# Kernel optimization log

Measured on AMD Instinct MI355X. Metric: run time of the kernel, lower is better.

## Reference

```python
import jax, jax.numpy as jnp
import numpy as np

NR, K = 175, 250              # num_ranges, top_k
N = NR * K                    # 43750 active radar points
SHAPE0 = (56, 350, 512)       # (ele, range, azi) full-res sparse grid
SHAPE1 = (28, 175, 256)       # after stride-2 sparse conv
SHAPE2 = (14, 88, 128)        # after second stride-2 sparse conv
CAP1 = 350000                 # <= 8*N unique active cells after stride-2 conv
CAP2 = 69000                  # reachable region bound at stage 2 (14*88*56)
BC = 16                       # base_channel
C1, C2, CO = 2 * BC, 8 * BC, 128
OFFS = [(a, b, c) for a in range(3) for b in range(3) for c in range(3)]


def bn(x, p):
    # BatchNorm1d (eval form): p = [gamma, beta, running_mean, running_var]
    g, b, m, v = p
    return (x - m) * jax.lax.rsqrt(v + 1e-3) * g + b


def gn(x, groups, gamma, beta):
    n, c = x.shape
    xr = x.reshape(n, groups, c // groups)
    m = xr.mean(-1, keepdims=True)
    v = ((xr - m) ** 2).mean(-1, keepdims=True)
    return ((xr - m) * jax.lax.rsqrt(v + 1e-5)).reshape(n, c) * gamma + beta


def build_lut(coords, shape, n):
    # dense coord -> row-index map; out-of-bounds (padded) coords are dropped
    lut = jnp.full(shape, -1, jnp.int32)
    return lut.at[coords[:, 0], coords[:, 1], coords[:, 2]].set(jnp.arange(n, dtype=jnp.int32), mode='drop')


def subm_conv(feats, coords, lut, shape, w):
    # submanifold 3x3x3 conv: outputs only at active sites (gather-GEMM-accumulate)
    S = jnp.array(shape, jnp.int32)
    out = jnp.zeros((feats.shape[0], w.shape[-1]), feats.dtype)
    for k, off in enumerate(OFFS):
        nb = coords + (jnp.array(off, jnp.int32) - 1)
        inb = jnp.all((nb >= 0) & (nb < S), axis=-1)
        nbc = jnp.clip(nb, 0, S - 1)
        idx = lut[nbc[:, 0], nbc[:, 1], nbc[:, 2]]
        ok = inb & (idx >= 0)
        f = jnp.where(ok[:, None], feats[jnp.maximum(idx, 0)], 0.0)
        out = out + f @ w[k]
    return out


def down_conv(feats, coords_in, lut_in, shape_in, shape_out, cap, w):
    # SparseConv3d k=3 stride=2 pad=1: output sites = cells with any active input in receptive field
    mask = jnp.zeros(shape_in, bool).at[coords_in[:, 0], coords_in[:, 1], coords_in[:, 2]].set(True, mode='drop')
    pm = jnp.pad(mask, 1)
    om = jnp.zeros(shape_out, bool)
    for (a, b, c) in OFFS:
        om = om | pm[a:a + 2 * shape_out[0]:2, b:b + 2 * shape_out[1]:2, c:c + 2 * shape_out[2]:2]
    i0, i1, i2 = jnp.nonzero(om, size=cap, fill_value=0)
    oc = jnp.stack([i0, i1, i2], -1).astype(jnp.int32)
    valid = jnp.arange(cap) < om.sum()
    S = jnp.array(shape_in, jnp.int32)
    out = jnp.zeros((cap, w.shape[-1]), feats.dtype)
    for k, off in enumerate(OFFS):
        nb = 2 * oc + (jnp.array(off, jnp.int32) - 1)   # input coord = 2j + k - 1
        inb = jnp.all((nb >= 0) & (nb < S), axis=-1)
        nbc = jnp.clip(nb, 0, S - 1)
        idx = lut_in[nbc[:, 0], nbc[:, 1], nbc[:, 2]]
        ok = inb & (idx >= 0)
        f = jnp.where(ok[:, None], feats[jnp.maximum(idx, 0)], 0.0)
        out = out + f @ w[k]
    # padded (invalid) rows get out-of-bounds coords so later scatters/luts drop them
    oc_safe = jnp.where(valid[:, None], oc, jnp.array(shape_out, jnp.int32))
    return out, oc_safe


def basic_block(f, coords, lut, shape, w2, p2):
    h = jax.nn.relu(bn(subm_conv(f, coords, lut, shape, w2[0]), p2[0]))
    h = bn(subm_conv(h, coords, lut, shape, w2[1]), p2[1])
    return jax.nn.relu(h + f)


def range_attn(pw, c1, c3, ele_table, azi_table, wq, bq, wk, bk, wv, bv):
    x = pw.reshape(NR, K, 1)
    e = ele_table[c1.reshape(NR, K)]   # [NR,K,3]
    a = azi_table[c3.reshape(NR, K)]   # [NR,K,3]
    scale = 32.0 ** -0.5               # queries.size(-1) = hidden_dim = 32
    for l in range(4):
        xin = jnp.concatenate([x, e, a], -1)           # [NR,K,7]
        q = xin @ wq[l] + bq[l]
        kk = xin @ wk[l] + bk[l]
        v = xin @ wv[l] + bv[l]
        att = jax.nn.softmax(jnp.einsum('rkd,rjd->rkj', q, kk) * scale, axis=-1)
        x = jnp.einsum('rkj,rjd->rkd', att, v)         # [NR,K,1]
    return x.reshape(N, 1)


def forward(voxel_features, coors, ele_table, azi_table, wq, bq, wk, bk, wv, bv,
            w_in, b_in, gin_g, gin_b, w_d1, bn_d1, w_r1, bn_r1,
            w_d2, bn_d2, w_r2, bn_r2, w_out, b_out, gout_g, gout_b):
    c1, c2, c3 = coors[:, 1], coors[:, 2], coors[:, 3]
    pw = jnp.log10(voxel_features[:, -2])[:, None]
    f_att = range_attn(pw, c1, c3, ele_table, azi_table, wq, bq, wk, bk, wv, bv)
    ele = c1 * 2 - 9          # (56 - 37*2)//2 = -9
    rng = c2 * 2
    azi = c3 * 2 + 149        # (512 - 107*2)//2 = 149
    feats = jnp.concatenate([ele[:, None].astype(jnp.float32), rng[:, None].astype(jnp.float32),
                             azi[:, None].astype(jnp.float32), f_att], -1)   # [N,4]
    coords0 = jnp.stack([ele, rng, azi], -1).astype(jnp.int32)
    # conv_input: 1x1x1 SubMConv (per-point linear) + GroupNorm(8) + ReLU
    f0 = jax.nn.relu(gn(feats @ w_in + b_in, 8, gin_g, gin_b))
    lut0 = build_lut(coords0, SHAPE0, N)
    f1, oc1 = down_conv(f0, coords0, lut0, SHAPE0, SHAPE1, CAP1, w_d1)
    f1 = jax.nn.relu(bn(f1, bn_d1))
    lut1 = build_lut(oc1, SHAPE1, CAP1)
    f1 = basic_block(f1, oc1, lut1, SHAPE1, w_r1[0], bn_r1[0])
    f1 = basic_block(f1, oc1, lut1, SHAPE1, w_r1[1], bn_r1[1])
    f2, oc2 = down_conv(f1, oc1, lut1, SHAPE1, SHAPE2, CAP2, w_d2)
    f2 = jax.nn.relu(bn(f2, bn_d2))
    lut2 = build_lut(oc2, SHAPE2, CAP2)
    f2 = basic_block(f2, oc2, lut2, SHAPE2, w_r2[0], bn_r2[0])
    f2 = basic_block(f2, oc2, lut2, SHAPE2, w_r2[1], bn_r2[1])
    # conv_out: SubMConv3d(k=3, bias) + GroupNorm(16) + ReLU
    fo = subm_conv(f2, oc2, lut2, SHAPE2, w_out) + b_out
    fo = jax.nn.relu(gn(fo, 16, gout_g, gout_b))
    dense = jnp.zeros(SHAPE2 + (CO,), fo.dtype).at[oc2[:, 0], oc2[:, 1], oc2[:, 2]].set(fo, mode='drop')
    # torch dense: [1,C,ele,range,azi].permute(0,1,4,3,2) -> [1,C,azi,range,ele]
    return jnp.transpose(dense, (3, 2, 1, 0))[None]


def setup_inputs():
    key = jax.random.key(0)
    ks = iter(jax.random.split(key, 64))
    nrm = lambda shp, s: jax.random.normal(next(ks), shp, jnp.float32) * s

    def bnp(c):
        return jnp.stack([1.0 + nrm((c,), 0.1), nrm((c,), 0.1), nrm((c,), 0.05),
                          1.0 + 0.1 * jax.random.uniform(next(ks), (c,), jnp.float32)])

    voxel_features = jax.random.uniform(next(ks), (N, 2), jnp.float32, 0.1, 100.0)
    c0 = jnp.zeros((N,), jnp.int32)
    c1 = jax.random.randint(next(ks), (N,), 5, 33, jnp.int32)      # ele bin -> ele_ind in [1,55]
    c2 = jnp.repeat(jnp.arange(NR, dtype=jnp.int32), K)            # 250 points per range bin
    c3 = jax.random.randint(next(ks), (N,), 0, 107, jnp.int32)
    coors = jnp.stack([c0, c1, c2, c3], -1)
    return dict(
        voxel_features=voxel_features, coors=coors, batch_size=1,
        ele_table=nrm((37, 3), 1.0), azi_table=nrm((107, 3), 1.0),
        wq=nrm((4, 7, 32), 0.3), bq=nrm((4, 32), 0.1),
        wk=nrm((4, 7, 32), 0.3), bk=nrm((4, 32), 0.1),
        wv=nrm((4, 7, 1), 0.3), bv=nrm((4, 1), 0.1),
        w_in=nrm((4, BC), 0.5), b_in=nrm((BC,), 0.1),
        gin_g=1.0 + nrm((BC,), 0.1), gin_b=nrm((BC,), 0.1),
        w_d1=nrm((27, BC, C1), (27 * BC) ** -0.5), bn_d1=bnp(C1),
        w_r1=nrm((2, 2, 27, C1, C1), (27 * C1) ** -0.5),
        bn_r1=jnp.stack([jnp.stack([bnp(C1), bnp(C1)]), jnp.stack([bnp(C1), bnp(C1)])]),
        w_d2=nrm((27, C1, C2), (27 * C1) ** -0.5), bn_d2=bnp(C2),
        w_r2=nrm((2, 2, 27, C2, C2), (27 * C2) ** -0.5),
        bn_r2=jnp.stack([jnp.stack([bnp(C2), bnp(C2)]), jnp.stack([bnp(C2), bnp(C2)])]),
        w_out=nrm((27, C2, CO), (27 * C2) ** -0.5), b_out=nrm((CO,), 0.1),
        gout_g=1.0 + nrm((CO,), 0.1), gout_b=nrm((CO,), 0.1),
    )


def reference(voxel_features, coors, batch_size, ele_table, azi_table, wq, bq, wk, bk, wv, bv,
              w_in, b_in, gin_g, gin_b, w_d1, bn_d1, w_r1, bn_r1,
              w_d2, bn_d2, w_r2, bn_r2, w_out, b_out, gout_g, gout_b):
    assert batch_size == 1
    return forward(voxel_features, coors, ele_table, azi_table, wq, bq, wk, bk, wv, bv,
                   w_in, b_in, gin_g, gin_b, w_d1, bn_d1, w_r1, bn_r1,
                   w_d2, bn_d2, w_r2, bn_r2, w_out, b_out, gout_g, gout_b)
```

## Files before the change

### kernel.cpp

```cpp
#include <hip/hip_runtime.h>
#include <math.h>

#define NRR 175
#define KK 250
#define NN (NRR*KK)

#define S0_0 56
#define S0_1 350
#define S0_2 512
#define S1_0 28
#define S1_1 175
#define S1_2 256
#define S2_0 14
#define S2_1 88
#define S2_2 128
#define CAP1 350000
#define CAP2 69000
#define C1 32
#define C2 128
#define FOP 69632
#define NB2X 69120

#define CELLS0 (S0_0*S0_1*S0_2)
#define CELLS1 (S1_0*S1_1*S1_2)
#define CELLS2 (S2_0*S2_1*S2_2)

#define ATT_SCALE 0.17677669529663687f

typedef __attribute__((ext_vector_type(8))) __bf16 bf16x8;
typedef __attribute__((ext_vector_type(16))) float f32x16;

typedef __attribute__((address_space(3))) unsigned int       lds_u32;
typedef const __attribute__((address_space(1))) unsigned int glb_u32;

__device__ __forceinline__ void gld_lds16(unsigned short* lds_base, const unsigned short* gptr) {
    __builtin_amdgcn_global_load_lds((glb_u32*)gptr, (lds_u32*)lds_base, 16, 0, 0);
}

__device__ __forceinline__ unsigned short f2b(float x) {
    unsigned int u = __builtin_bit_cast(unsigned int, x);
    unsigned int r = u + 0x7FFFu + ((u >> 16) & 1u);
    return (unsigned short)(r >> 16);
}
__device__ __forceinline__ float b2f(unsigned short h) {
    return __builtin_bit_cast(float, (unsigned int)h << 16);
}

__device__ __forceinline__ int xcd_swizzle(int b, int nx) {
    int per = nx >> 3, rem = nx & 7;
    int x = b & 7, i = b >> 3;
    return x * per + min(x, rem) + i;
}

__device__ __forceinline__ int block_incl_scan(int v, int* s) {
    int t = threadIdx.x;
    s[t] = v; __syncthreads();
    #pragma unroll
    for (int d = 1; d < 256; d <<= 1) {
        int x = (t >= d) ? s[t - d] : 0;
        __syncthreads();
        s[t] += x;
        __syncthreads();
    }
    return s[t];
}

__device__ __forceinline__ void cand(int p, int So, int* o, int& no) {
    no = 0;
    if ((p & 1) == 0) {
        int q = p >> 1; if (q < So) o[no++] = q;
    } else {
        int q = (p - 1) >> 1; if (q < So) o[no++] = q;
        q = (p + 1) >> 1;     if (q < So) o[no++] = q;
    }
}

__global__ __launch_bounds__(256) void k_init(const float* __restrict__ vf,
                                              const int* __restrict__ coors,
                                              float* __restrict__ x,
                                              int* __restrict__ lut0,
                                              int* __restrict__ om1) {
    int i = blockIdx.x * 256 + threadIdx.x;
    if (i >= NN) return;
    x[i] = log10f(vf[i * 2]);
    int c1 = coors[i * 4 + 1], c2 = coors[i * 4 + 2], c3 = coors[i * 4 + 3];
    int e = 2 * c1 - 9, rg = 2 * c2, az = 2 * c3 + 149;
    atomicMax(&lut0[(e * S0_1 + rg) * S0_2 + az], i);
    int A[2], B[2], C[2]; int na, nb, nc;
    cand(e, S1_0, A, na); cand(rg, S1_1, B, nb); cand(az, S1_2, C, nc);
    for (int ia = 0; ia < na; ia++)
        for (int ib = 0; ib < nb; ib++)
            for (int ic = 0; ic < nc; ic++)
                om1[(A[ia] * S1_1 + B[ib]) * S1_2 + C[ic]] = 1;
}

#define QS 40
__global__ __launch_bounds__(256, 1) void k_attn(float* __restrict__ x_io,
    const int* __restrict__ coors,
    const float* __restrict__ et, const float* __restrict__ at,
    const float* __restrict__ wq, const float* __restrict__ bq,
    const float* __restrict__ wk, const float* __restrict__ bk,
    const float* __restrict__ wv, const float* __restrict__ bv) {
    __shared__ float xin[KK * 7];
    __shared__ unsigned short ksh_h[256 * QS];
    __shared__ unsigned short ksh_l[256 * QS];
    __shared__ float vsh[256];
    const int r = blockIdx.x;
    const int t = threadIdx.x;
    const int w = t >> 6, ln = t & 63, l31 = ln & 31, lh = ln >> 5;

    for (int i = t; i < KK; i += 256) {
        int gi = r * KK + i;
        xin[i * 7 + 0] = x_io[gi];
        int c1 = coors[gi * 4 + 1], c3 = coors[gi * 4 + 3];
        xin[i * 7 + 1] = et[c1 * 3 + 0]; xin[i * 7 + 2] = et[c1 * 3 + 1]; xin[i * 7 + 3] = et[c1 * 3 + 2];
        xin[i * 7 + 4] = at[c3 * 3 + 0]; xin[i * 7 + 5] = at[c3 * 3 + 1]; xin[i * 7 + 6] = at[c3 * 3 + 2];
    }
    __syncthreads();

    union U8 { bf16x8 v; unsigned short u[8]; };

    for (int l = 0; l < 4; l++) {
        const float* wql = wq + l * 7 * 32; const float* bql = bq + l * 32;
        const float* wkl = wk + l * 7 * 32; const float* bkl = bk + l * 32;
        const float* wvl = wv + l * 7;      const float  bvl = bv[l];
        float qh_f[32], ql_f[32];
        if (t < KK) {
            float xi[7];
            #pragma unroll
            for (int ci = 0; ci < 7; ci++) xi[ci] = xin[t * 7 + ci];
            float av = bvl;
            #pragma unroll
            for (int ci = 0; ci < 7; ci++) av += xi[ci] * wvl[ci];
            vsh[t] = av;
            #pragma unroll
            for (int d = 0; d < 32; d++) {
                float aq = bql[d], ak = bkl[d];
                #pragma unroll
                for (int ci = 0; ci < 7; ci++) { aq += xi[ci] * wql[ci * 32 + d]; ak += xi[ci] * wkl[ci * 32 + d]; }
                aq *= ATT_SCALE;
                float h = b2f(f2b(aq));
                qh_f[d] = h; ql_f[d] = aq - h;
                unsigned short k16 = f2b(ak);
                ksh_h[t * QS + d] = k16;
                ksh_l[t * QS + d] = f2b(ak - b2f(k16));
            }
        } else {
            #pragma unroll
            for (int d = 0; d < 32; d++) {
                qh_f[d] = 0.f; ql_f[d] = 0.f;
                ksh_h[t * QS + d] = 0; ksh_l[t * QS + d] = 0;
            }
            vsh[t] = 0.f;
        }
        __syncthreads();

        U8 Bh[2][2], Bl[2][2];
        #pragma unroll
        for (int b = 0; b < 2; b++) {
            int src = b * 32 + l31;
            #pragma unroll
            for (int ks = 0; ks < 2; ks++) {
                #pragma unroll
                for (int j = 0; j < 8; j++) {
                    float h0 = __shfl(qh_f[ks * 16 + j],     src, 64);
                    float h1 = __shfl(qh_f[ks * 16 + 8 + j], src, 64);
                    float l0 = __shfl(ql_f[ks * 16 + j],     src, 64);
                    float l1 = __shfl(ql_f[ks * 16 + 8 + j], src, 64);
                    Bh[b][ks].u[j] = f2b(lh ? h1 : h0);
                    Bl[b][ks].u[j] = f2b(lh ? l1 : l0);
                }
            }
        }

        float m[2]  = {-1e30f, -1e30f};
        float den[2] = {0.f, 0.f};
        float num[2] = {0.f, 0.f};

        for (int mt = 0; mt < 8; mt++) {
            U8 Ah[2], Al[2];
            int krow = mt * 32 + l31;
            #pragma unroll
            for (int ks = 0; ks < 2; ks++) {
                Ah[ks].v = *(const bf16x8*)&ksh_h[krow * QS + ks * 16 + lh * 8];
                Al[ks].v = *(const bf16x8*)&ksh_l[krow * QS + ks * 16 + lh * 8];
            }
            float4 v4[4];
            #pragma unroll
            for (int c = 0; c < 4; c++)
                v4[c] = *(const float4*)&vsh[mt * 32 + 8 * c + 4 * lh];

            #pragma unroll
            for (int b = 0; b < 2; b++) {
                f32x16 acc;
                #pragma unroll
                for (int q = 0; q < 16; q++) acc[q] = 0.f;
                acc = __builtin_amdgcn_mfma_f32_32x32x16_bf16(Ah[0].v, Bh[b][0].v, acc, 0, 0, 0);
                acc = __builtin_amdgcn_mfma_f32_32x32x16_bf16(Ah[1].v, Bh[b][1].v, acc, 0, 0, 0);
                acc = __builtin_amdgcn_mfma_f32_32x32x16_bf16(Ah[0].v, Bl[b][0].v, acc, 0, 0, 0);
                acc = __builtin_amdgcn_mfma_f32_32x32x16_bf16(Ah[1].v, Bl[b][1].v, acc, 0, 0, 0);
                acc = __builtin_amdgcn_mfma_f32_32x32x16_bf16(Al[0].v, Bh[b][0].v, acc, 0, 0, 0);
                acc = __builtin_amdgcn_mfma_f32_32x32x16_bf16(Al[1].v, Bh[b][1].v, acc, 0, 0, 0);

                float s[16];
                #pragma unroll
                for (int rr = 0; rr < 16; rr++) {
                    s[rr] = acc[rr];
                    if (mt == 7) {
                        int key = 224 + (rr & 3) + 8 * (rr >> 2) + 4 * lh;
                        if (key >= KK) s[rr] = -1e30f;
                    }
                }
                float cm = s[0];
                #pragma unroll
                for (int rr = 1; rr < 16; rr++) cm = fmaxf(cm, s[rr]);
                cm = fmaxf(cm, __shfl_xor(cm, 32, 64));
                float mn = fmaxf(m[b], cm);
                float alpha = __expf(m[b] - mn);
                float dsum = 0.f, nsum = 0.f;
                #pragma unroll
                for (int rr = 0; rr < 16; rr++) {
                    float e = __expf(s[rr] - mn);
                    dsum += e;
                    nsum += e * ((&v4[rr >> 2].x)[rr & 3]);
                }
                den[b] = den[b] * alpha + dsum;
                num[b] = num[b] * alpha + nsum;
                m[b] = mn;
            }
        }
        __syncthreads();
        #pragma unroll
        for (int b = 0; b < 2; b++) {
            float dtot = den[b] + __shfl_xor(den[b], 32, 64);
            float ntot = num[b] + __shfl_xor(num[b], 32, 64);
            int q = (w * 2 + b) * 32 + l31;
            if (lh == 0 && q < KK) xin[q * 7] = ntot / dtot;
        }
        __syncthreads();
    }
    for (int i = t; i < KK; i += 256) x_io[r * KK + i] = xin[i * 7];
}

__global__ __launch_bounds__(256) void k_f0(const int* __restrict__ coors,
    const float* __restrict__ x,
    const float* __restrict__ w_in, const float* __restrict__ b_in,
    const float* __restrict__ gg, const float* __restrict__ gb,
    unsigned short* __restrict__ f0) {
    int i = blockIdx.x * 256 + threadIdx.x;
    if (i >= NN) return;
    int c1 = coors[i * 4 + 1], c2 = coors[i * 4 + 2], c3 = coors[i * 4 + 3];
    float fe0 = (float)(2 * c1 - 9), fe1 = (float)(2 * c2), fe2 = (float)(2 * c3 + 149), fe3 = x[i];
    float tv[16];
    #pragma unroll
    for (int c = 0; c < 16; c++)
        tv[c] = b_in[c] + fe0 * w_in[c] + fe1 * w_in[16 + c] + fe2 * w_in[32 + c] + fe3 * w_in[48 + c];
    #pragma unroll
    for (int g = 0; g < 8; g++) {
        float a = tv[2 * g], b = tv[2 * g + 1];
        float m = 0.5f * (a + b);
        float va = 0.5f * ((a - m) * (a - m) + (b - m) * (b - m));
        float inv = rsqrtf(va + 1e-5f);
        f0[i * 16 + 2 * g]     = f2b(fmaxf((a - m) * inv * gg[2 * g]     + gb[2 * g],     0.f));
        f0[i * 16 + 2 * g + 1] = f2b(fmaxf((b - m) * inv * gg[2 * g + 1] + gb[2 * g + 1], 0.f));
    }
}

__global__ __launch_bounds__(256) void k_blocksum(const int* __restrict__ om,
                                                  int* __restrict__ partials, int ncells) {
    __shared__ int sh[256];
    int t = threadIdx.x;
    int base = blockIdx.x * 1024 + t * 4;
    int s = 0;
    #pragma unroll
    for (int q = 0; q < 4; q++) s += (base + q < ncells) ? om[base + q] : 0;
    int incl = block_incl_scan(s, sh);
    if (t == 255) partials[blockIdx.x] = incl;
}

__global__ __launch_bounds__(256) void k_scanparts(int* __restrict__ partials, int nparts,
                                                   int* __restrict__ pcnt, int cap) {
    __shared__ int sh[256];
    __shared__ int tot;
    int t = threadIdx.x;
    int chunk = (nparts + 255) / 256;
    int beg = t * chunk;
    int vals[8];
    int s = 0;
    #pragma unroll
    for (int i = 0; i < 8; i++) {
        if (i < chunk) {
            int ix = beg + i;
            int x = (ix < nparts) ? partials[ix] : 0;
            vals[i] = x; s += x;
        }
    }
    int incl = block_incl_scan(s, sh);
    int excl = incl - s;
    if (t == 255) tot = incl;
    int run = excl;
    #pragma unroll
    for (int i = 0; i < 8; i++) {
        if (i < chunk) {
            int ix = beg + i;
            if (ix < nparts) { partials[ix] = run; run += vals[i]; }
        }
    }
    __syncthreads();
    if (t == 0) *pcnt = min(tot, cap);
}

__global__ __launch_bounds__(256) void k_emit(const int* __restrict__ om,
                                              const int* __restrict__ partials,
                                              int* __restrict__ oc,
                                              int ncells, int D1, int D2, int cap) {
    __shared__ int sh[256];
    int t = threadIdx.x;
    int base = blockIdx.x * 1024 + t * 4;
    int v[4]; int s = 0;
    #pragma unroll
    for (int q = 0; q < 4; q++) { v[q] = (base + q < ncells) ? om[base + q] : 0; s += v[q]; }
    int incl = block_incl_scan(s, sh);
    int run = partials[blockIdx.x] + (incl - s);
    int D12 = D1 * D2;
    #pragma unroll
    for (int q = 0; q < 4; q++) {
        if (v[q]) {
            if (run < cap) {
                int lin = base + q;
                int i0 = lin / D12;
                int r2 = lin - i0 * D12;
                int i1 = r2 / D2;
                int i2 = r2 - i1 * D2;
                oc[run * 3] = i0; oc[run * 3 + 1] = i1; oc[run * 3 + 2] = i2;
            }
            run++;
        }
    }
}

__global__ __launch_bounds__(256) void k_lutscatter(const int* __restrict__ oc,
                                                    const int* __restrict__ pc,
                                                    int* __restrict__ lut, int D1, int D2) {
    int j = blockIdx.x * 256 + threadIdx.x;
    if (j >= *pc) return;
    lut[(oc[j * 3] * D1 + oc[j * 3 + 1]) * D2 + oc[j * 3 + 2]] = j;
}

__global__ __launch_bounds__(256) void k_lutscatter2(const int* __restrict__ oc,
                                                     const int* __restrict__ pc,
                                                     int* __restrict__ lut,
                                                     int* __restrict__ lut_t) {
    int j = blockIdx.x * 256 + threadIdx.x;
    if (j >= *pc) return;
    int a = oc[j * 3], b = oc[j * 3 + 1], c = oc[j * 3 + 2];
    lut[(a * S2_1 + b) * S2_2 + c] = j;
    lut_t[(c * S2_1 + b) * S2_0 + a] = j;
}

__global__ __launch_bounds__(256) void k_mask2(const int* __restrict__ oc,
                                               const int* __restrict__ pc,
                                               int* __restrict__ om) {
    int j = blockIdx.x * 256 + threadIdx.x;
    if (j >= *pc) return;
    int p0 = oc[j * 3], p1 = oc[j * 3 + 1], p2 = oc[j * 3 + 2];
    int A[2], B[2], C[2]; int na, nb, nc;
    cand(p0, S2_0, A, na); cand(p1, S2_1, B, nb); cand(p2, S2_2, C, nc);
    for (int ia = 0; ia < na; ia++)
        for (int ib = 0; ib < nb; ib++)
            for (int ic = 0; ic < nc; ic++)
                om[(A[ia] * S2_1 + B[ib]) * S2_2 + C[ic]] = 1;
}

__global__ __launch_bounds__(256) void k_prepack(const float* __restrict__ w,
        unsigned short* __restrict__ wp, int nk, int cin, int cout) {
    int tid = blockIdx.x * 256 + threadIdx.x;
    int tot = nk * cin * cout;
    if (tid >= tot) return;
    int co = tid % cout; int rest = tid / cout; int ci = rest % cin; int kk = rest / cin;
    int ks = ci >> 4, kr = ci & 15, half = kr >> 3, j = kr & 7;
    int nt = co >> 5, cl = co & 31, lane = half * 32 + cl;
    wp[((((size_t)kk * (cin >> 4) + ks) * (cout >> 5) + nt) * 64 + lane) * 8 + j] = f2b(w[tid]);
}

template<bool DOWN, int SD0, int SD1, int SD2>
__global__ __launch_bounds__(256) void k_nbidx(const int* __restrict__ oc,
        const int* __restrict__ pc, const int* __restrict__ lut,
        int* __restrict__ nb, int NBx, int ZR) {
    int gid = blockIdx.x * 256 + threadIdx.x;
    if (gid >= 27 * NBx) return;
    int k = gid / NBx, j = gid - k * NBx;
    int idx = ZR;
    if (j < *pc) {
        int dx = k / 9 - 1, dy = (k / 3) % 3 - 1, dz = k % 3 - 1;
        int x = oc[j * 3], y = oc[j * 3 + 1], z = oc[j * 3 + 2];
        if (DOWN) { x = 2 * x + dx; y = 2 * y + dy; z = 2 * z + dz; }
        else      { x += dx; y += dy; z += dz; }
        if ((unsigned)x < (unsigned)SD0 && (unsigned)y < (unsigned)SD1 && (unsigned)z < (unsigned)SD2) {
            int v = lut[(x * SD1 + y) * SD2 + z];
            if (v >= 0) idx = v;
        }
    }
    nb[gid] = idx;
}

template<int CIN, int COUT, int SD0, int SD1, int SD2, bool DOWN, int MODE, bool TAB>
__global__ __launch_bounds__(256, 2)
void k_aconv(const unsigned short* __restrict__ fin, const int* __restrict__ lut,
             const int* __restrict__ nb, int NBx,
             const int* __restrict__ oc, const int* __restrict__ pc,
             const unsigned short* __restrict__ wp,
             const float* __restrict__ p0, const float* __restrict__ p1,
             const float* __restrict__ p2,
             const unsigned short* __restrict__ res, void* __restrict__ fout_,
             int ZR) {
    constexpr int KS  = CIN / 16;
    constexpr int NTT = COUT / 32;
    constexpr int TM  = (COUT == 128) ? 4 : 1;
    constexpr int CPR = CIN / 8;
    constexpr int RPI = 64 / CPR;
    constexpr int IPW = 32 / RPI;
    constexpr int SH  = (CPR == 16) ? 0 : ((CPR == 4) ? 1 : 2);
    __shared__ unsigned short sA[2 * 128 * CIN];

    const int n = *pc;
    const int blk = xcd_swizzle(blockIdx.x, gridDim.x);
    const int j0 = blk * 128;
    if (j0 >= n) return;
    const int t = threadIdx.x;
    const int w = t >> 6, ln = t & 63, l31 = ln & 31, lh = ln >> 5;
    const int rowb = (COUT == 128) ? 0 : w * 32;
    const int colt = (COUT == 128) ? w : 0;

    const int lrow = ln / CPR;
    const int slot = ln % CPR;
    int myrow[IPW];
    #pragma unroll
    for (int i = 0; i < IPW; i++) myrow[i] = w * 32 + i * RPI + lrow;

    int cxa[IPW], cya[IPW], cza[IPW];
    if (!TAB) {
        #pragma unroll
        for (int i = 0; i < IPW; i++) {
            int j = j0 + myrow[i];
            if (j < n) { cxa[i] = oc[j * 3]; cya[i] = oc[j * 3 + 1]; cza[i] = oc[j * 3 + 2]; }
            else       { cxa[i] = -1000000; cya[i] = -1000000; cza[i] = -1000000; }
        }
    }

    auto fetchIdx = [&](int kk, int* ir) {
        if (TAB) {
            #pragma unroll
            for (int i = 0; i < IPW; i++)
                ir[i] = nb[kk * NBx + j0 + myrow[i]];
        } else {
            int dx = kk / 9 - 1, dy = (kk / 3) % 3 - 1, dz = kk % 3 - 1;
            #pragma unroll
            for (int i = 0; i < IPW; i++) {
                int x, y, z;
                if (DOWN) { x = 2 * cxa[i] + dx; y = 2 * cya[i] + dy; z = 2 * cza[i] + dz; }
                else      { x = cxa[i] + dx; y = cya[i] + dy; z = cza[i] + dz; }
                int idx = -1;
                if ((unsigned)x < (unsigned)SD0 && (unsigned)y < (unsigned)SD1 && (unsigned)z < (unsigned)SD2)
                    idx = lut[(x * SD1 + y) * SD2 + z];
                ir[i] = idx < 0 ? ZR : idx;
            }
        }
    };

    auto stage = [&](int buf, const int* ir) {
        #pragma unroll
        for (int i = 0; i < IPW; i++) {
            unsigned short* ldsb = &sA[(size_t)buf * 128 * CIN + (w * 32 + i * RPI) * CIN];
            int g = (myrow[i] >> SH) & (CPR - 1);
            const unsigned short* gp = fin + (size_t)ir[i] * CIN + ((slot ^ g) * 8);
            gld_lds16(ldsb, gp);
        }
    };

    f32x16 acc[TM];
    #pragma unroll
    for (int a = 0; a < TM; a++)
        #pragma unroll
        for (int q = 0; q < 16; q++) acc[a][q] = 0.f;

    int irn[IPW];
    fetchIdx(0, irn);
    stage(0, irn);
    fetchIdx(1, irn);

    for (int k = 0; k < 27; k++) {
        __syncthreads();
        if (k < 26) {
            stage((k + 1) & 1, irn);
            fetchIdx(k + 2 <= 26 ? k + 2 : 26, irn);
        }
        const unsigned short* wk = wp + (size_t)k * KS * NTT * 512;
        const unsigned short* bufA = &sA[(size_t)(k & 1) * 128 * CIN];
        #pragma unroll
        for (int ks = 0; ks < KS; ks++) {
            bf16x8 bfr = *(const bf16x8*)(wk + ((size_t)(ks * NTT + colt) * 64 + ln) * 8);
            #pragma unroll
            for (int a = 0; a < TM; a++) {
                int r = rowb + a * 32 + l31;
                int c = ks * 2 + lh;
                int sl = c ^ ((r >> SH) & (CPR - 1));
                bf16x8 afr = *(const bf16x8*)(bufA + (size_t)r * CIN + sl * 8);
                acc[a] = __builtin_amdgcn_mfma_f32_32x32x16_bf16(afr, bfr, acc[a], 0, 0, 0);
            }
        }
    }

    const int co = colt * 32 + l31;
    if (MODE != 2) {
        unsigned short* fout = (unsigned short*)fout_;
        float g_ = p0[co], bb_ = p0[COUT + co], m_ = p0[2 * COUT + co];
        float iv = rsqrtf(p0[3 * COUT + co] + 1e-3f);
        #pragma unroll
        for (int a = 0; a < TM; a++) {
            #pragma unroll
            for (int r = 0; r < 16; r++) {
                int j = j0 + rowb + a * 32 + (r & 3) + 8 * (r >> 2) + 4 * lh;
                if (j < n) {
                    float y = (acc[a][r] - m_) * iv * g_ + bb_;
                    if (MODE == 1) y += b2f(res[(size_t)j * COUT + co]);
                    fout[(size_t)j * COUT + co] = f2b(fmaxf(y, 0.f));
                }
            }
        }
    } else {
        float* fo_t = (float*)fout_;
        float bias = p0[co], gg_ = p1[co], gb_ = p2[co];
        #pragma unroll
        for (int a = 0; a < TM; a++) {
            #pragma unroll
            for (int r = 0; r < 16; r++) {
                int j = j0 + rowb + a * 32 + (r & 3) + 8 * (r >> 2) + 4 * lh;
                float y = acc[a][r] + bias;
                float s = y;
                s += __shfl_xor(s, 1, 8);
                s += __shfl_xor(s, 2, 8);
                s += __shfl_xor(s, 4, 8);
                float m = s * 0.125f;
                float d = y - m;
                float q2 = d * d;
                q2 += __shfl_xor(q2, 1, 8);
                q2 += __shfl_xor(q2, 2, 8);
                q2 += __shfl_xor(q2, 4, 8);
                float var = q2 * 0.125f;
                float o = fmaxf(d * rsqrtf(var + 1e-5f) * gg_ + gb_, 0.f);
                fo_t[(size_t)co * FOP + j] = o;
            }
        }
    }
}

__global__ __launch_bounds__(256) void k_scatter(const float* __restrict__ fo_t,
                                                 const int* __restrict__ lut2t,
                                                 float* __restrict__ dout) {
    int gid = blockIdx.x * 256 + threadIdx.x;
    int cell = gid % CELLS2;
    int co = gid / CELLS2;
    int idx = lut2t[cell];
    float v = 0.f;
    if (idx >= 0) v = fo_t[(size_t)co * FOP + idx];
    dout[gid] = v;
}

extern "C" void kernel_launch(void* const* d_in, const int* in_sizes, int n_in,
                              void* d_out, int out_size, void* d_ws, size_t ws_size,
                              hipStream_t stream) {
    const float* vf    = (const float*)d_in[0];
    const int*   coors = (const int*)d_in[1];
    const float* et    = (const float*)d_in[3];
    const float* at    = (const float*)d_in[4];
    const float* wq    = (const float*)d_in[5];
    const float* bq    = (const float*)d_in[6];
    const float* wk_   = (const float*)d_in[7];
    const float* bk    = (const float*)d_in[8];
    const float* wv    = (const float*)d_in[9];
    const float* bv    = (const float*)d_in[10];
    const float* w_in  = (const float*)d_in[11];
    const float* b_in  = (const float*)d_in[12];
    const float* gin_g = (const float*)d_in[13];
    const float* gin_b = (const float*)d_in[14];
    const float* w_d1  = (const float*)d_in[15];
    const float* bn_d1 = (const float*)d_in[16];
    const float* w_r1  = (const float*)d_in[17];
    const float* bn_r1 = (const float*)d_in[18];
    const float* w_d2  = (const float*)d_in[19];
    const float* bn_d2 = (const float*)d_in[20];
    const float* w_r2  = (const float*)d_in[21];
    const float* bn_r2 = (const float*)d_in[22];
    const float* w_out = (const float*)d_in[23];
    const float* b_out = (const float*)d_in[24];
    const float* gout_g= (const float*)d_in[25];
    const float* gout_b= (const float*)d_in[26];

    char* ws = (char*)d_ws;
    size_t cur = 0;
    auto take = [&](size_t bytes) -> char* {
        char* p = ws + cur;
        cur += (bytes + 255) & ~(size_t)255;
        return p;
    };
    size_t usz1 = (size_t)4194304 + (size_t)CELLS0 * 4;
    size_t usz2 = (size_t)17694720 + (size_t)128 * FOP * 4;
    char* U = take(usz1 > usz2 ? usz1 : usz2);
    float*          x_att = (float*)U;
    unsigned short* f0    = (unsigned short*)(U + 262144);
    int*            lut0  = (int*)(U + 4194304);
    unsigned short* fB1   = (unsigned short*)U;
    unsigned short* fA2   = (unsigned short*)U;
    unsigned short* fB2   = (unsigned short*)(U + 17694720);
    float*          fo_t  = (float*)(U + 17694720);

    int*   om1      = (int*)take((size_t)CELLS1 * 4);
    int*   om2      = (int*)take((size_t)CELLS2 * 4);
    int*   partials = (int*)take(8192);
    int*   cnt      = (int*)take(256);
    int*   oc1      = (int*)take((size_t)CAP1 * 3 * 4);
    int*   oc2      = (int*)take((size_t)CAP2 * 3 * 4);
    unsigned short* fA1 = (unsigned short*)take((size_t)(CAP1 + 1) * C1 * 2);
    int*   lut1     = (int*)take((size_t)CELLS1 * 4);
    int*   lut2     = (int*)take((size_t)CELLS2 * 4);
    int*   lut2t    = (int*)take((size_t)CELLS2 * 4);
    int*   nb_d2    = (int*)take((size_t)27 * NB2X * 4);
    int*   nb_r2    = (int*)take((size_t)27 * NB2X * 4);
    unsigned short* wp_d1  = (unsigned short*)take((size_t)27 * 16 * 32 * 2);
    unsigned short* wp_r1  = (unsigned short*)take((size_t)108 * 32 * 32 * 2);
    unsigned short* wp_d2  = (unsigned short*)take((size_t)27 * 32 * 128 * 2);
    unsigned short* wp_r2  = (unsigned short*)take((size_t)108 * 128 * 128 * 2);
    unsigned short* wp_out = (unsigned short*)take((size_t)27 * 128 * 128 * 2);

    hipMemsetAsync(lut0, 0xFF, (size_t)CELLS0 * 4, stream);
    hipMemsetAsync(om1, 0, (size_t)CELLS1 * 4, stream);
    hipMemsetAsync(om2, 0, (size_t)CELLS2 * 4, stream);
    hipMemsetAsync(lut1, 0xFF, (size_t)CELLS1 * 4, stream);
    hipMemsetAsync(lut2, 0xFF, (size_t)CELLS2 * 4, stream);
    hipMemsetAsync(lut2t, 0xFF, (size_t)CELLS2 * 4, stream);
    hipMemsetAsync(f0 + (size_t)NN * 16, 0, 32, stream);
    hipMemsetAsync(fA1 + (size_t)CAP1 * C1, 0, 64, stream);

    const int gN  = (NN + 255) / 256;
    const int gB1 = CELLS1 / 1024;
    const int gB2 = CELLS2 / 1024;
    const int gM1 = (CAP1 + 127) / 128;
    const int gM2 = (CAP2 + 127) / 128;
    const int gS1 = (CAP1 + 255) / 256;
    const int gS2 = (CAP2 + 255) / 256;
    const int gNB = (27 * NB2X + 255) / 256;

    k_prepack<<<(27*16*32   + 255)/256, 256, 0, stream>>>(w_d1,  wp_d1, 27, 16, 32);
    k_prepack<<<(108*32*32  + 255)/256, 256, 0, stream>>>(w_r1,  wp_r1, 108, 32, 32);
    k_prepack<<<(27*32*128  + 255)/256, 256, 0, stream>>>(w_d2,  wp_d2, 27, 32, 128);
    k_prepack<<<(108*128*128+ 255)/256, 256, 0, stream>>>(w_r2,  wp_r2, 108, 128, 128);
    k_prepack<<<(27*128*128 + 255)/256, 256, 0, stream>>>(w_out, wp_out, 27, 128, 128);

    k_init<<<gN, 256, 0, stream>>>(vf, coors, x_att, lut0, om1);
    k_attn<<<NRR, 256, 0, stream>>>(x_att, coors, et, at, wq, bq, wk_, bk, wv, bv);
    k_f0<<<gN, 256, 0, stream>>>(coors, x_att, w_in, b_in, gin_g, gin_b, f0);

    k_blocksum<<<gB1, 256, 0, stream>>>(om1, partials, CELLS1);
    k_scanparts<<<1, 256, 0, stream>>>(partials, gB1, cnt, CAP1);
    k_emit<<<gB1, 256, 0, stream>>>(om1, partials, oc1, CELLS1, S1_1, S1_2, CAP1);

    k_aconv<16, 32, S0_0, S0_1, S0_2, true, 0, false><<<gM1, 256, 0, stream>>>(
        f0, lut0, nullptr, 0, oc1, cnt, wp_d1, bn_d1, nullptr, nullptr, nullptr, fA1, NN);
    k_lutscatter<<<gS1, 256, 0, stream>>>(oc1, cnt, lut1, S1_1, S1_2);
    hipMemsetAsync(fB1 + (size_t)CAP1 * C1, 0, 64, stream);

    k_aconv<32, 32, S1_0, S1_1, S1_2, false, 0, false><<<gM1, 256, 0, stream>>>(
        fA1, lut1, nullptr, 0, oc1, cnt, wp_r1 + 0 * 27648, bn_r1 + 0 * 128, nullptr, nullptr, nullptr, fB1, CAP1);
    k_aconv<32, 32, S1_0, S1_1, S1_2, false, 1, false><<<gM1, 256, 0, stream>>>(
        fB1, lut1, nullptr, 0, oc1, cnt, wp_r1 + 1 * 27648, bn_r1 + 1 * 128, nullptr, nullptr, fA1, fA1, CAP1);
    k_aconv<32, 32, S1_0, S1_1, S1_2, false, 0, false><<<gM1, 256, 0, stream>>>(
        fA1, lut1, nullptr, 0, oc1, cnt, wp_r1 + 2 * 27648, bn_r1 + 2 * 128, nullptr, nullptr, nullptr, fB1, CAP1);
    k_aconv<32, 32, S1_0, S1_1, S1_2, false, 1, false><<<gM1, 256, 0, stream>>>(
        fB1, lut1, nullptr, 0, oc1, cnt, wp_r1 + 3 * 27648, bn_r1 + 3 * 128, nullptr, nullptr, fA1, fA1, CAP1);

    k_mask2<<<gS1, 256, 0, stream>>>(oc1, cnt, om2);
    k_blocksum<<<gB2, 256, 0, stream>>>(om2, partials, CELLS2);
    k_scanparts<<<1, 256, 0, stream>>>(partials, gB2, cnt + 1, CAP2);
    k_emit<<<gB2, 256, 0, stream>>>(om2, partials, oc2, CELLS2, S2_1, S2_2, CAP2);

    k_nbidx<true, S1_0, S1_1, S1_2><<<gNB, 256, 0, stream>>>(oc2, cnt + 1, lut1, nb_d2, NB2X, CAP1);
    hipMemsetAsync(fA2 + (size_t)CAP2 * C2, 0, 256, stream);
    hipMemsetAsync(fB2 + (size_t)CAP2 * C2, 0, 256, stream);

    k_aconv<32, 128, S1_0, S1_1, S1_2, true, 0, true><<<gM2, 256, 0, stream>>>(
        fA1, nullptr, nb_d2, NB2X, oc2, cnt + 1, wp_d2, bn_d2, nullptr, nullptr, nullptr, fA2, CAP1);
    k_lutscatter2<<<gS2, 256, 0, stream>>>(oc2, cnt + 1, lut2, lut2t);
    k_nbidx<false, S2_0, S2_1, S2_2><<<gNB, 256, 0, stream>>>(oc2, cnt + 1, lut2, nb_r2, NB2X, CAP2);

    const size_t wr2s = (size_t)27 * 128 * 128;
    k_aconv<128, 128, S2_0, S2_1, S2_2, false, 0, true><<<gM2, 256, 0, stream>>>(
        fA2, nullptr, nb_r2, NB2X, oc2, cnt + 1, wp_r2 + 0 * wr2s, bn_r2 + 0 * 512, nullptr, nullptr, nullptr, fB2, CAP2);
    k_aconv<128, 128, S2_0, S2_1, S2_2, false, 1, true><<<gM2, 256, 0, stream>>>(
        fB2, nullptr, nb_r2, NB2X, oc2, cnt + 1, wp_r2 + 1 * wr2s, bn_r2 + 1 * 512, nullptr, nullptr, fA2, fA2, CAP2);
    k_aconv<128, 128, S2_0, S2_1, S2_2, false, 0, true><<<gM2, 256, 0, stream>>>(
        fA2, nullptr, nb_r2, NB2X, oc2, cnt + 1, wp_r2 + 2 * wr2s, bn_r2 + 2 * 512, nullptr, nullptr, nullptr, fB2, CAP2);
    k_aconv<128, 128, S2_0, S2_1, S2_2, false, 1, true><<<gM2, 256, 0, stream>>>(
        fB2, nullptr, nb_r2, NB2X, oc2, cnt + 1, wp_r2 + 3 * wr2s, bn_r2 + 3 * 512, nullptr, nullptr, fA2, fA2, CAP2);

    k_aconv<128, 128, S2_0, S2_1, S2_2, false, 2, true><<<gM2, 256, 0, stream>>>(
        fA2, nullptr, nb_r2, NB2X, oc2, cnt + 1, wp_out, b_out, gout_g, gout_b, nullptr, fo_t, CAP2);
    k_scatter<<<(S2_0 * S2_1 * S2_2 * 128) / 256, 256, 0, stream>>>(fo_t, lut2t, (float*)d_out);
}
```

Before: 1.329 ms.

## Use 512-thread blocks with configurable row tile and preload weight fragments

The active-site conv kernel now runs with 8 waves per block. Its row tile is a template parameter: 256 rows for the stage-1 convs and 128 rows for stage-2, where waves split rows across two groups and each handles two 32-row MFMA tiles. The per-tap weight fragments are loaded into registers before the next gather is issued, so those loads overlap the staging. This aims to raise occupancy and latency hiding for the gather-bound GEMMs, at the cost of a new launch-bounds register limit and a larger LDS footprint for the 256-row blocks.

```diff
diff --git a/kernel.cpp b/kernel.cpp
--- a/kernel.cpp
+++ b/kernel.cpp
@@ -404,8 +404,8 @@
     nb[gid] = idx;
 }
 
-template<int CIN, int COUT, int SD0, int SD1, int SD2, bool DOWN, int MODE, bool TAB>
-__global__ __launch_bounds__(256, 2)
+template<int CIN, int COUT, int ROWS, int SD0, int SD1, int SD2, bool DOWN, int MODE, bool TAB>
+__global__ __launch_bounds__(512, 4)
 void k_aconv(const unsigned short* __restrict__ fin, const int* __restrict__ lut,
              const int* __restrict__ nb, int NBx,
              const int* __restrict__ oc, const int* __restrict__ pc,
@@ -416,27 +416,29 @@
              int ZR) {
     constexpr int KS  = CIN / 16;
     constexpr int NTT = COUT / 32;
-    constexpr int TM  = (COUT == 128) ? 4 : 1;
+    constexpr int NRG = 8 / NTT;
+    constexpr int TM  = (ROWS / 32) / NRG;
     constexpr int CPR = CIN / 8;
     constexpr int RPI = 64 / CPR;
-    constexpr int IPW = 32 / RPI;
+    constexpr int RPW = ROWS / 8;
+    constexpr int IPW = RPW / RPI;
     constexpr int SH  = (CPR == 16) ? 0 : ((CPR == 4) ? 1 : 2);
-    __shared__ unsigned short sA[2 * 128 * CIN];
+    __shared__ unsigned short sA[2 * ROWS * CIN];
 
     const int n = *pc;
     const int blk = xcd_swizzle(blockIdx.x, gridDim.x);
-    const int j0 = blk * 128;
+    const int j0 = blk * ROWS;
     if (j0 >= n) return;
     const int t = threadIdx.x;
     const int w = t >> 6, ln = t & 63, l31 = ln & 31, lh = ln >> 5;
-    const int rowb = (COUT == 128) ? 0 : w * 32;
-    const int colt = (COUT == 128) ? w : 0;
+    const int colt = w & (NTT - 1);
+    const int rowb = (w / NTT) * TM * 32;
 
     const int lrow = ln / CPR;
     const int slot = ln % CPR;
     int myrow[IPW];
     #pragma unroll
-    for (int i = 0; i < IPW; i++) myrow[i] = w * 32 + i * RPI + lrow;
+    for (int i = 0; i < IPW; i++) myrow[i] = w * RPW + i * RPI + lrow;
 
     int cxa[IPW], cya[IPW], cza[IPW];
     if (!TAB) {
@@ -471,7 +473,7 @@
     auto stage = [&](int buf, const int* ir) {
         #pragma unroll
         for (int i = 0; i < IPW; i++) {
-            unsigned short* ldsb = &sA[(size_t)buf * 128 * CIN + (w * 32 + i * RPI) * CIN];
+            unsigned short* ldsb = &sA[(size_t)buf * ROWS * CIN + (w * RPW + i * RPI) * CIN];
             int g = (myrow[i] >> SH) & (CPR - 1);
             const unsigned short* gp = fin + (size_t)ir[i] * CIN + ((slot ^ g) * 8);
             gld_lds16(ldsb, gp);
@@ -491,22 +493,25 @@
 
     for (int k = 0; k < 27; k++) {
         __syncthreads();
+        const unsigned short* wk = wp + (size_t)k * KS * NTT * 512;
+        bf16x8 breg[KS];
+        #pragma unroll
+        for (int ks = 0; ks < KS; ks++)
+            breg[ks] = *(const bf16x8*)(wk + ((size_t)(ks * NTT + colt) * 64 + ln) * 8);
         if (k < 26) {
             stage((k + 1) & 1, irn);
             fetchIdx(k + 2 <= 26 ? k + 2 : 26, irn);
         }
-        const unsigned short* wk = wp + (size_t)k * KS * NTT * 512;
-        const unsigned short* bufA = &sA[(size_t)(k & 1) * 128 * CIN];
+        const unsigned short* bufA = &sA[(size_t)(k & 1) * ROWS * CIN];
         #pragma unroll
         for (int ks = 0; ks < KS; ks++) {
-            bf16x8 bfr = *(const bf16x8*)(wk + ((size_t)(ks * NTT + colt) * 64 + ln) * 8);
             #pragma unroll
             for (int a = 0; a < TM; a++) {
                 int r = rowb + a * 32 + l31;
                 int c = ks * 2 + lh;
                 int sl = c ^ ((r >> SH) & (CPR - 1));
                 bf16x8 afr = *(const bf16x8*)(bufA + (size_t)r * CIN + sl * 8);
-                acc[a] = __builtin_amdgcn_mfma_f32_32x32x16_bf16(afr, bfr, acc[a], 0, 0, 0);
+                acc[a] = __builtin_amdgcn_mfma_f32_32x32x16_bf16(afr, breg[ks], acc[a], 0, 0, 0);
             }
         }
     }
@@ -645,7 +650,7 @@
     const int gN  = (NN + 255) / 256;
     const int gB1 = CELLS1 / 1024;
     const int gB2 = CELLS2 / 1024;
-    const int gM1 = (CAP1 + 127) / 128;
+    const int gM1 = (CAP1 + 255) / 256;
     const int gM2 = (CAP2 + 127) / 128;
     const int gS1 = (CAP1 + 255) / 256;
     const int gS2 = (CAP2 + 255) / 256;
@@ -665,18 +670,18 @@
     k_scanparts<<<1, 256, 0, stream>>>(partials, gB1, cnt, CAP1);
     k_emit<<<gB1, 256, 0, stream>>>(om1, partials, oc1, CELLS1, S1_1, S1_2, CAP1);
 
-    k_aconv<16, 32, S0_0, S0_1, S0_2, true, 0, false><<<gM1, 256, 0, stream>>>(
+    k_aconv<16, 32, 256, S0_0, S0_1, S0_2, true, 0, false><<<gM1, 512, 0, stream>>>(
         f0, lut0, nullptr, 0, oc1, cnt, wp_d1, bn_d1, nullptr, nullptr, nullptr, fA1, NN);
     k_lutscatter<<<gS1, 256, 0, stream>>>(oc1, cnt, lut1, S1_1, S1_2);
     hipMemsetAsync(fB1 + (size_t)CAP1 * C1, 0, 64, stream);
 
-    k_aconv<32, 32, S1_0, S1_1, S1_2, false, 0, false><<<gM1, 256, 0, stream>>>(
+    k_aconv<32, 32, 256, S1_0, S1_1, S1_2, false, 0, false><<<gM1, 512, 0, stream>>>(
         fA1, lut1, nullptr, 0, oc1, cnt, wp_r1 + 0 * 27648, bn_r1 + 0 * 128, nullptr, nullptr, nullptr, fB1, CAP1);
-    k_aconv<32, 32, S1_0, S1_1, S1_2, false, 1, false><<<gM1, 256, 0, stream>>>(
+    k_aconv<32, 32, 256, S1_0, S1_1, S1_2, false, 1, false><<<gM1, 512, 0, stream>>>(
         fB1, lut1, nullptr, 0, oc1, cnt, wp_r1 + 1 * 27648, bn_r1 + 1 * 128, nullptr, nullptr, fA1, fA1, CAP1);
-    k_aconv<32, 32, S1_0, S1_1, S1_2, false, 0, false><<<gM1, 256, 0, stream>>>(
+    k_aconv<32, 32, 256, S1_0, S1_1, S1_2, false, 0, false><<<gM1, 512, 0, stream>>>(
         fA1, lut1, nullptr, 0, oc1, cnt, wp_r1 + 2 * 27648, bn_r1 + 2 * 128, nullptr, nullptr, nullptr, fB1, CAP1);
-    k_aconv<32, 32, S1_0, S1_1, S1_2, false, 1, false><<<gM1, 256, 0, stream>>>(
+    k_aconv<32, 32, 256, S1_0, S1_1, S1_2, false, 1, false><<<gM1, 512, 0, stream>>>(
         fB1, lut1, nullptr, 0, oc1, cnt, wp_r1 + 3 * 27648, bn_r1 + 3 * 128, nullptr, nullptr, fA1, fA1, CAP1);
 
     k_mask2<<<gS1, 256, 0, stream>>>(oc1, cnt, om2);
@@ -688,22 +693,22 @@
     hipMemsetAsync(fA2 + (size_t)CAP2 * C2, 0, 256, stream);
     hipMemsetAsync(fB2 + (size_t)CAP2 * C2, 0, 256, stream);
 
-    k_aconv<32, 128, S1_0, S1_1, S1_2, true, 0, true><<<gM2, 256, 0, stream>>>(
+    k_aconv<32, 128, 128, S1_0, S1_1, S1_2, true, 0, true><<<gM2, 512, 0, stream>>>(
         fA1, nullptr, nb_d2, NB2X, oc2, cnt + 1, wp_d2, bn_d2, nullptr, nullptr, nullptr, fA2, CAP1);
     k_lutscatter2<<<gS2, 256, 0, stream>>>(oc2, cnt + 1, lut2, lut2t);
     k_nbidx<false, S2_0, S2_1, S2_2><<<gNB, 256, 0, stream>>>(oc2, cnt + 1, lut2, nb_r2, NB2X, CAP2);
 
     const size_t wr2s = (size_t)27 * 128 * 128;
-    k_aconv<128, 128, S2_0, S2_1, S2_2, false, 0, true><<<gM2, 256, 0, stream>>>(
+    k_aconv<128, 128, 128, S2_0, S2_1, S2_2, false, 0, true><<<gM2, 512, 0, stream>>>(
         fA2, nullptr, nb_r2, NB2X, oc2, cnt + 1, wp_r2 + 0 * wr2s, bn_r2 + 0 * 512, nullptr, nullptr, nullptr, fB2, CAP2);
-    k_aconv<128, 128, S2_0, S2_1, S2_2, false, 1, true><<<gM2, 256, 0, stream>>>(
+    k_aconv<128, 128, 128, S2_0, S2_1, S2_2, false, 1, true><<<gM2, 512, 0, stream>>>(
         fB2, nullptr, nb_r2, NB2X, oc2, cnt + 1, wp_r2 + 1 * wr2s, bn_r2 + 1 * 512, nullptr, nullptr, fA2, fA2, CAP2);
-    k_aconv<128, 128, S2_0, S2_1, S2_2, false, 0, true><<<gM2, 256, 0, stream>>>(
+    k_aconv<128, 128, 128, S2_0, S2_1, S2_2, false, 0, true><<<gM2, 512, 0, stream>>>(
         fA2, nullptr, nb_r2, NB2X, oc2, cnt + 1, wp_r2 + 2 * wr2s, bn_r2 + 2 * 512, nullptr, nullptr, nullptr, fB2, CAP2);
-    k_aconv<128, 128, S2_0, S2_1, S2_2, false, 1, true><<<gM2, 256, 0, stream>>>(
+    k_aconv<128, 128, 128, S2_0, S2_1, S2_2, false, 1, true><<<gM2, 512, 0, stream>>>(
         fB2, nullptr, nb_r2, NB2X, oc2, cnt + 1, wp_r2 + 3 * wr2s, bn_r2 + 3 * 512, nullptr, nullptr, fA2, fA2, CAP2);
 
-    k_aconv<128, 128, S2_0, S2_1, S2_2, false, 2, true><<<gM2, 256, 0, stream>>>(
+    k_aconv<128, 128, 128, S2_0, S2_1, S2_2, false, 2, true><<<gM2, 512, 0, stream>>>(
         fA2, nullptr, nb_r2, NB2X, oc2, cnt + 1, wp_out, b_out, gout_g, gout_b, nullptr, fo_t, CAP2);
     k_scatter<<<(S2_0 * S2_1 * S2_2 * 128) / 256, 256, 0, stream>>>(fo_t, lut2t, (float*)d_out);
 }
```

Result: faster. 1.210 ms (-9.0%).
